# Kernel optimization log

Hardware: AMD Instinct MI355X
Metric: run time of the kernel (lower is better)

## Reference

```python
import jax, jax.numpy as jnp
import numpy as np

C = 512
NUM_HEADS = 8
GROUPS = 32
EPS_GN = 1e-5
EPS_ATTN = 1e-6


def setup_inputs() -> dict:
    key = jax.random.key(0)
    ks = jax.random.split(key, 7)
    B, H, W = 8, 64, 64
    x = jax.random.normal(ks[0], (B, C, H, W), dtype=jnp.float32)
    # GroupNorm affine (torch default: weight=1, bias=0)
    norm_gamma = jnp.ones((C,), dtype=jnp.float32)
    norm_beta = jnp.zeros((C,), dtype=jnp.float32)
    # 1x1 conv weights stored as (out, in); torch Conv2d kaiming-ish scale
    qkv_w = jax.random.normal(ks[1], (3 * C, C), dtype=jnp.float32) * (1.0 / np.sqrt(C))
    qkv_b = jax.random.normal(ks[2], (3 * C,), dtype=jnp.float32) * 0.01
    proj_w = jax.random.normal(ks[3], (C, C), dtype=jnp.float32) * (1.0 / np.sqrt(C))
    proj_b = jax.random.normal(ks[4], (C,), dtype=jnp.float32) * 0.01
    return {"x": x, "norm_gamma": norm_gamma, "norm_beta": norm_beta,
            "qkv_w": qkv_w, "qkv_b": qkv_b, "proj_w": proj_w, "proj_b": proj_b}


def _group_norm(x, gamma, beta):
    B, Cc, H, W = x.shape
    xg = x.reshape(B, GROUPS, Cc // GROUPS, H, W)
    mean = xg.mean(axis=(2, 3, 4), keepdims=True)
    var = xg.var(axis=(2, 3, 4), keepdims=True)
    xn = (xg - mean) * jax.lax.rsqrt(var + EPS_GN)
    xn = xn.reshape(B, Cc, H, W)
    return xn * gamma[None, :, None, None] + beta[None, :, None, None]


def reference(x, norm_gamma, norm_beta, qkv_w, qkv_b, proj_w, proj_b):
    B, Cc, H, W = x.shape
    h, d = NUM_HEADS, Cc // NUM_HEADS
    N = H * W
    x_norm = _group_norm(x, norm_gamma, norm_beta)
    # 1x1 conv == channel GEMM
    qkv = jnp.einsum('bchw,oc->bohw', x_norm, qkv_w) + qkv_b[None, :, None, None]
    q, k, v = jnp.split(qkv, 3, axis=1)
    # (B, C, H, W) -> (B, h, N, d)
    def to_heads(t):
        return t.reshape(B, h, d, N).transpose(0, 1, 3, 2)
    q, k, v = to_heads(q), to_heads(k), to_heads(v)
    # phi(x) = elu(x) + 1
    q = jax.nn.elu(q) + 1.0
    k = jax.nn.elu(k) + 1.0
    kv = jnp.einsum('bhnd,bhne->bhde', k, v)          # (B,h,d,d)
    out = jnp.einsum('bhnd,bhde->bhne', q, kv)        # (B,h,N,d)
    denom = jnp.einsum('bhnd,bhd->bhn', q, k.sum(axis=2))
    out = out / (denom[..., None] + EPS_ATTN)
    # (B,h,N,d) -> (B,C,H,W)
    attn = out.transpose(0, 1, 3, 2).reshape(B, Cc, H, W)
    proj = jnp.einsum('bchw,oc->bohw', attn, proj_w) + proj_b[None, :, None, None]
    # dropout is identity at inference
    return x + proj
```

## Files before the change

### kernel.cpp

```cpp
#include <hip/hip_runtime.h>
#include <math.h>

#define BATCH   8
#define CCH     512
#define NHEADS  8
#define HD      64
#define NGROUPS 32
#define CPG     16
#define NSP     4096
#define O1      1536

typedef __attribute__((ext_vector_type(8))) short          short8;
typedef __attribute__((ext_vector_type(8))) unsigned short ushort8;
typedef __attribute__((ext_vector_type(4))) unsigned short ushort4v;
typedef __attribute__((ext_vector_type(4))) float          float4v;

#define GLOAD_LDS16(g, s) __builtin_amdgcn_global_load_lds(                   \
    (const __attribute__((address_space(1))) void*)(g),                       \
    (__attribute__((address_space(3))) void*)(s), 16, 0, 0)

__device__ __forceinline__ float phi_act(float v) {
    return v > 0.f ? v + 1.f : __expf(v);
}
__device__ __forceinline__ unsigned short f2bf(float f) {
    union { float f; unsigned int u; } c; c.f = f;
    unsigned int u = c.u;
    u += 0x7fffu + ((u >> 16) & 1u);
    return (unsigned short)(u >> 16);
}
__device__ __forceinline__ float bf2f(unsigned short s) {
    union { unsigned int u; float f; } c; c.u = ((unsigned int)s) << 16;
    return c.f;
}


__global__ __launch_bounds__(256) void pre_kernel(const float* __restrict__ x,
                                                  const float* __restrict__ gamma,
                                                  const float* __restrict__ beta,
                                                  const float* __restrict__ qw,
                                                  const float* __restrict__ pw,
                                                  unsigned short* __restrict__ qwb,
                                                  unsigned short* __restrict__ pwb,
                                                  float* __restrict__ ksum,
                                                  float* __restrict__ ss) {
    __shared__ float r1[256], r2[256];
    const int bid = blockIdx.x;
    const int t   = threadIdx.x;
    if (bid < 1024) {
        int i = (bid * 256 + t) * 4;
        if (i < O1 * CCH) {
            float4 v = *(const float4*)(qw + i);
            unsigned short o[4] = {f2bf(v.x), f2bf(v.y), f2bf(v.z), f2bf(v.w)};
            *(uint2*)(qwb + i) = *(uint2*)o;
        } else {
            int j = i - O1 * CCH;
            float4 v = *(const float4*)(pw + j);
            unsigned short o[4] = {f2bf(v.x), f2bf(v.y), f2bf(v.z), f2bf(v.w)};
            *(uint2*)(pwb + j) = *(uint2*)o;
        }
        if (bid == 0) {
            float4 z = {0.f, 0.f, 0.f, 0.f};
            #pragma unroll
            for (int l = 0; l < 4; ++l)
                *(float4*)(ksum + (l * 256 + t) * 4) = z;
        }
        return;
    }
    const int bg = bid - 1024;
    const float* base = x + (size_t)bg * (CPG * NSP);
    float s = 0.f, s2 = 0.f;
    #pragma unroll 4
    for (int i = 0; i < 64; ++i) {
        float4 v = *(const float4*)(base + (i * 256 + t) * 4);
        s  += v.x + v.y + v.z + v.w;
        s2 += v.x * v.x + v.y * v.y + v.z * v.z + v.w * v.w;
    }
    r1[t] = s; r2[t] = s2;
    __syncthreads();
    for (int off = 128; off > 0; off >>= 1) {
        if (t < off) { r1[t] += r1[t + off]; r2[t] += r2[t + off]; }
        __syncthreads();
    }
    if (t < CPG) {
        const float inv = 1.f / 65536.f;
        float mean = r1[0] * inv;
        float var  = r2[0] * inv - mean * mean;
        float rstd = rsqrtf(var + 1e-5f);
        int b = bg / NGROUPS, g = bg % NGROUPS;
        int c = g * CPG + t;
        float sc = gamma[c] * rstd;
        float sh = beta[c] - mean * sc;
        ss[(b * CCH + c) * 2]     = sc;
        ss[(b * CCH + c) * 2 + 1] = sh;
    }
}

__global__ __launch_bounds__(256) void xnT_kernel(const float* __restrict__ x,
                                                  const float* __restrict__ ss,
                                                  unsigned short* __restrict__ xnT) {
    const int n0 = blockIdx.x * 64, c0 = blockIdx.y * 64, b = blockIdx.z;
    const int t = threadIdx.x;
    __shared__ float tile[64][65];
    const float* xb  = x + ((size_t)b * CCH + c0) * NSP + n0;
    const float* ssb = ss + b * CCH * 2;

    const int lr = t / 16, lc = (t % 16) * 4;
    #pragma unroll
    for (int j = 0; j < 4; ++j) {
        int cr = j * 16 + lr;
        float4 v = *(const float4*)(xb + (size_t)cr * NSP + lc);
        float sc = ssb[(c0 + cr) * 2], sh = ssb[(c0 + cr) * 2 + 1];
        tile[cr][lc + 0] = v.x * sc + sh;
        tile[cr][lc + 1] = v.y * sc + sh;
        tile[cr][lc + 2] = v.z * sc + sh;
        tile[cr][lc + 3] = v.w * sc + sh;
    }
    __syncthreads();
    #pragma unroll
    for (int j = 0; j < 2; ++j) {
        int wd = j * 256 + t;
        int n  = wd >> 3;
        int cb = (wd & 7) * 8;
        ushort8 o;
        #pragma unroll
        for (int i = 0; i < 8; ++i) o[i] = f2bf(tile[cb + i][n]);
        *(ushort8*)(xnT + ((size_t)b * NSP + n0 + n) * CCH + c0 + cb) = o;
    }
}

__global__ __launch_bounds__(256) void gemm_qkv(const unsigned short* __restrict__ A,
                                                const unsigned short* __restrict__ Bt,
                                                const float* __restrict__ bias,
                                                unsigned short* __restrict__ qT,
                                                float* __restrict__ ksum,
                                                float* __restrict__ kvp) {
    const int n0 = blockIdx.x * 128;
    const int b  = blockIdx.z;
    const int t  = threadIdx.x;
    const int wv = t >> 6, ln = t & 63;
    const int quad = ln >> 4, lm = ln & 15;
    const int wo = (wv >> 1) * 64, wn = (wv & 1) * 64;

    __shared__ __align__(16) unsigned short sh[16384];

    float4v acc[4][4];
    #pragma unroll
    for (int i = 0; i < 4; ++i)
        #pragma unroll
        for (int j = 0; j < 4; ++j) acc[i][j] = {0.f, 0.f, 0.f, 0.f};

    const unsigned short* bBase = Bt + ((size_t)b * NSP + n0) * CCH;
    const int srow = ln >> 2;
    const int scol = ((ln & 3) ^ ((ln >> 3) & 3)) * 8;
    const int slab0 = wv * 2, slab1 = slab0 + 1;
    const int dA0 = slab0 * 512, dA1 = slab1 * 512;
    const int sc  = (quad ^ ((lm >> 1) & 3)) * 8;

    if (blockIdx.y < 8) {
        const int h = blockIdx.y;
        const unsigned short* aK = A + (size_t)(512 + h * 64) * CCH;
        const unsigned short* aV = A + (size_t)(1024 + h * 64) * CCH;
        const unsigned short* aR0 = ((slab0 < 4)
            ? aK + (size_t)(slab0 * 16 + srow) * CCH
            : aV + (size_t)((slab0 - 4) * 16 + srow) * CCH) + scol;
        const unsigned short* aR1 = ((slab1 < 4)
            ? aK + (size_t)(slab1 * 16 + srow) * CCH
            : aV + (size_t)((slab1 - 4) * 16 + srow) * CCH) + scol;
        const unsigned short* bR0 = bBase + (size_t)(slab0 * 16 + srow) * CCH + scol;
        const unsigned short* bR1 = bBase + (size_t)(slab1 * 16 + srow) * CCH + scol;

        GLOAD_LDS16(aR0, sh + dA0);
        GLOAD_LDS16(aR1, sh + dA1);
        GLOAD_LDS16(bR0, sh + 4096 + dA0);
        GLOAD_LDS16(bR1, sh + 4096 + dA1);
        __syncthreads();

        int cur = 0;
        for (int step = 0; step < 15; ++step) {
            const int nb = (cur ^ 1) * 8192;
            const int k1 = (step + 1) * 32;
            GLOAD_LDS16(aR0 + k1, sh + nb + dA0);
            GLOAD_LDS16(aR1 + k1, sh + nb + dA1);
            GLOAD_LDS16(bR0 + k1, sh + nb + 4096 + dA0);
            GLOAD_LDS16(bR1 + k1, sh + nb + 4096 + dA1);
            const unsigned short* Ab = sh + cur * 8192;
            const unsigned short* Bb = Ab + 4096;
            short8 fw[4], fx[4];
            #pragma unroll
            for (int i = 0; i < 4; ++i)
                fw[i] = *(const short8*)(Ab + (wo + i * 16 + lm) * 32 + sc);
            #pragma unroll
            for (int j = 0; j < 4; ++j)
                fx[j] = *(const short8*)(Bb + (wn + j * 16 + lm) * 32 + sc);
            #pragma unroll
            for (int i = 0; i < 4; ++i)
                #pragma unroll
                for (int j = 0; j < 4; ++j)
                    acc[i][j] = __builtin_amdgcn_mfma_f32_16x16x32_bf16(
                        fx[j], fw[i], acc[i][j], 0, 0, 0);
            __syncthreads();
            cur ^= 1;
        }
        {
            const unsigned short* Ab = sh + cur * 8192;
            const unsigned short* Bb = Ab + 4096;
            short8 fw[4], fx[4];
            #pragma unroll
            for (int i = 0; i < 4; ++i)
                fw[i] = *(const short8*)(Ab + (wo + i * 16 + lm) * 32 + sc);
            #pragma unroll
            for (int j = 0; j < 4; ++j)
                fx[j] = *(const short8*)(Bb + (wn + j * 16 + lm) * 32 + sc);
            #pragma unroll
            for (int i = 0; i < 4; ++i)
                #pragma unroll
                for (int j = 0; j < 4; ++j)
                    acc[i][j] = __builtin_amdgcn_mfma_f32_16x16x32_bf16(
                        fx[j], fw[i], acc[i][j], 0, 0, 0);
        }

        __syncthreads();
        const bool isk = (wv < 2);
        const float* bptr = bias + (isk ? 512 : 1024) + h * 64;
        float ksp[4] = {0.f, 0.f, 0.f, 0.f};
        #pragma unroll
        for (int i = 0; i < 4; ++i) {
            float bs = bptr[i * 16 + lm];
            int row = wo + i * 16 + lm;
            #pragma unroll
            for (int j = 0; j < 4; ++j) {
                int n = wn + j * 16 + quad * 4;
                ushort4v pk;
                #pragma unroll
                for (int r = 0; r < 4; ++r) {
                    float v = acc[i][j][r] + bs;
                    if (isk) { v = phi_act(v); ksp[i] += v; }
                    pk[r] = f2bf(v);
                }
                int idx = row * 128 + ((((n >> 3) ^ (row & 15)) << 3) | (n & 7));
                *(ushort4v*)(sh + idx) = pk;
            }
        }
        if (isk) {
            #pragma unroll
            for (int i = 0; i < 4; ++i) {
                float s = ksp[i];
                s += __shfl_xor(s, 16);
                s += __shfl_xor(s, 32);
                if (quad == 0)
                    atomicAdd(ksum + b * CCH + h * 64 + i * 16 + lm, s);
            }
        }
        __syncthreads();

        const int wd = (wv >> 1) * 32, we = (wv & 1) * 32;
        float4v acc2[2][2];
        #pragma unroll
        for (int i = 0; i < 2; ++i)
            #pragma unroll
            for (int j = 0; j < 2; ++j) acc2[i][j] = {0.f, 0.f, 0.f, 0.f};

        #pragma unroll
        for (int ks = 0; ks < 4; ++ks) {
            short8 ka[2], vbf[2];
            #pragma unroll
            for (int i2 = 0; i2 < 2; ++i2) {
                int row = wd + i2 * 16 + lm;
                ka[i2] = *(const short8*)(sh + row * 128 +
                                          (((ks * 4 + quad) ^ (row & 15)) << 3));
            }
            #pragma unroll
            for (int j2 = 0; j2 < 2; ++j2) {
                int row = 64 + we + j2 * 16 + lm;
                vbf[j2] = *(const short8*)(sh + row * 128 +
                                           (((ks * 4 + quad) ^ (row & 15)) << 3));
            }
            #pragma unroll
            for (int i2 = 0; i2 < 2; ++i2)
                #pragma unroll
                for (int j2 = 0; j2 < 2; ++j2)
                    acc2[i2][j2] = __builtin_amdgcn_mfma_f32_16x16x32_bf16(
                        vbf[j2], ka[i2], acc2[i2][j2], 0, 0, 0);
        }

        const int chunk = blockIdx.x;
        const int bh = b * 8 + h;
        #pragma unroll
        for (int i2 = 0; i2 < 2; ++i2)
            #pragma unroll
            for (int j2 = 0; j2 < 2; ++j2) {
                int d = wd + i2 * 16 + lm;
                int e = we + j2 * 16 + quad * 4;
                float4 r = {acc2[i2][j2][0], acc2[i2][j2][1],
                            acc2[i2][j2][2], acc2[i2][j2][3]};
                *(float4*)(kvp + ((size_t)(chunk * 64 + bh) * 64 + d) * 64 + e) = r;
            }
    } else {
        const int o0 = (blockIdx.y - 8) * 128;
        const unsigned short* aBase = A + (size_t)o0 * CCH;
        const unsigned short* aR0 = aBase + (size_t)(slab0 * 16 + srow) * CCH + scol;
        const unsigned short* aR1 = aBase + (size_t)(slab1 * 16 + srow) * CCH + scol;
        const unsigned short* bR0 = bBase + (size_t)(slab0 * 16 + srow) * CCH + scol;
        const unsigned short* bR1 = bBase + (size_t)(slab1 * 16 + srow) * CCH + scol;

        GLOAD_LDS16(aR0, sh + dA0);
        GLOAD_LDS16(aR1, sh + dA1);
        GLOAD_LDS16(bR0, sh + 4096 + dA0);
        GLOAD_LDS16(bR1, sh + 4096 + dA1);
        __syncthreads();

        int cur = 0;
        for (int step = 0; step < 15; ++step) {
            const int nb = (cur ^ 1) * 8192;
            const int k1 = (step + 1) * 32;
            GLOAD_LDS16(aR0 + k1, sh + nb + dA0);
            GLOAD_LDS16(aR1 + k1, sh + nb + dA1);
            GLOAD_LDS16(bR0 + k1, sh + nb + 4096 + dA0);
            GLOAD_LDS16(bR1 + k1, sh + nb + 4096 + dA1);
            const unsigned short* Ab = sh + cur * 8192;
            const unsigned short* Bb = Ab + 4096;
            short8 fw[4], fx[4];
            #pragma unroll
            for (int i = 0; i < 4; ++i)
                fw[i] = *(const short8*)(Ab + (wo + i * 16 + lm) * 32 + sc);
            #pragma unroll
            for (int j = 0; j < 4; ++j)
                fx[j] = *(const short8*)(Bb + (wn + j * 16 + lm) * 32 + sc);
            #pragma unroll
            for (int i = 0; i < 4; ++i)
                #pragma unroll
                for (int j = 0; j < 4; ++j)
                    acc[i][j] = __builtin_amdgcn_mfma_f32_16x16x32_bf16(
                        fw[i], fx[j], acc[i][j], 0, 0, 0);
            __syncthreads();
            cur ^= 1;
        }
        {
            const unsigned short* Ab = sh + cur * 8192;
            const unsigned short* Bb = Ab + 4096;
            short8 fw[4], fx[4];
            #pragma unroll
            for (int i = 0; i < 4; ++i)
                fw[i] = *(const short8*)(Ab + (wo + i * 16 + lm) * 32 + sc);
            #pragma unroll
            for (int j = 0; j < 4; ++j)
                fx[j] = *(const short8*)(Bb + (wn + j * 16 + lm) * 32 + sc);
            #pragma unroll
            for (int i = 0; i < 4; ++i)
                #pragma unroll
                for (int j = 0; j < 4; ++j)
                    acc[i][j] = __builtin_amdgcn_mfma_f32_16x16x32_bf16(
                        fw[i], fx[j], acc[i][j], 0, 0, 0);
        }

        #pragma unroll
        for (int i = 0; i < 4; ++i) {
            int ob = o0 + wo + i * 16 + quad * 4;
            float4 b4 = *(const float4*)(bias + ob);
            float bs[4] = {b4.x, b4.y, b4.z, b4.w};
            #pragma unroll
            for (int j = 0; j < 4; ++j) {
                int n = n0 + wn + j * 16 + lm;
                ushort4v pk;
                #pragma unroll
                for (int r = 0; r < 4; ++r)
                    pk[r] = f2bf(phi_act(acc[i][j][r] + bs[r]));
                *(ushort4v*)(qT + ((size_t)b * NSP + n) * CCH + ob) = pk;
            }
        }
    }
}

__global__ __launch_bounds__(256) void post_kernel(const float* __restrict__ kvp,
                                                   const unsigned short* __restrict__ pwb,
                                                   const unsigned short* __restrict__ qT,
                                                   const float* __restrict__ ksum,
                                                   unsigned short* __restrict__ Mw,
                                                   float* __restrict__ den) {
    const int t = threadIdx.x;
    __shared__ __align__(16) unsigned short kvs[64 * 64];

    if (blockIdx.x < 64) {
        const int bh = blockIdx.x;
        const int b = bh >> 3, h = bh & 7;
        const int wv = t >> 6, ln = t & 63;
        const int quad = ln >> 4, lm = ln & 15;

        {
            const int d = t >> 2, e0 = (t & 3) * 16;
            float4 s0 = {0.f, 0.f, 0.f, 0.f}, s1 = s0, s2 = s0, s3 = s0;
            for (int p = 0; p < 32; ++p) {
                const float* src = kvp + ((size_t)(p * 64 + bh) * 64 + d) * 64 + e0;
                float4 v0 = *(const float4*)(src);
                float4 v1 = *(const float4*)(src + 4);
                float4 v2 = *(const float4*)(src + 8);
                float4 v3 = *(const float4*)(src + 12);
                s0.x += v0.x; s0.y += v0.y; s0.z += v0.z; s0.w += v0.w;
                s1.x += v1.x; s1.y += v1.y; s1.z += v1.z; s1.w += v1.w;
                s2.x += v2.x; s2.y += v2.y; s2.z += v2.z; s2.w += v2.w;
                s3.x += v3.x; s3.y += v3.y; s3.z += v3.z; s3.w += v3.w;
            }
            ushort8 o0 = {f2bf(s0.x), f2bf(s0.y), f2bf(s0.z), f2bf(s0.w),
                          f2bf(s1.x), f2bf(s1.y), f2bf(s1.z), f2bf(s1.w)};
            ushort8 o1 = {f2bf(s2.x), f2bf(s2.y), f2bf(s2.z), f2bf(s2.w),
                          f2bf(s3.x), f2bf(s3.y), f2bf(s3.z), f2bf(s3.w)};
            int c0 = e0 >> 3;
            *(ushort8*)(kvs + d * 64 + ((c0 ^ (d & 7)) << 3))       = o0;
            *(ushort8*)(kvs + d * 64 + (((c0 + 1) ^ (d & 7)) << 3)) = o1;
        }
        __syncthreads();

        short8 ka[4][2];
        #pragma unroll
        for (int i = 0; i < 4; ++i)
            #pragma unroll
            for (int kk = 0; kk < 2; ++kk) {
                int d = i * 16 + lm;
                ka[i][kk] = *(const short8*)(kvs + d * 64 +
                            (((kk * 4 + quad) ^ (lm & 7)) << 3));
            }
        for (int half = 0; half < 2; ++half) {
            const int ob = half * 256 + wv * 64;
            short8 fw[4][2];
            #pragma unroll
            for (int j = 0; j < 4; ++j)
                #pragma unroll
                for (int kk = 0; kk < 2; ++kk) {
                    int o = ob + j * 16 + lm;
                    fw[j][kk] = *(const short8*)(pwb + (size_t)o * CCH + h * 64 +
                                                 kk * 32 + quad * 8);
                }
            float4v acc[4][4];
            #pragma unroll
            for (int i = 0; i < 4; ++i)
                #pragma unroll
                for (int j = 0; j < 4; ++j) acc[i][j] = {0.f, 0.f, 0.f, 0.f};
            #pragma unroll
            for (int kk = 0; kk < 2; ++kk)
                #pragma unroll
                for (int i = 0; i < 4; ++i)
                    #pragma unroll
                    for (int j = 0; j < 4; ++j)
                        acc[i][j] = __builtin_amdgcn_mfma_f32_16x16x32_bf16(
                            ka[i][kk], fw[j][kk], acc[i][j], 0, 0, 0);
            #pragma unroll
            for (int i = 0; i < 4; ++i)
                #pragma unroll
                for (int j = 0; j < 4; ++j) {
                    int o = ob + j * 16 + lm;
                    int c = h * 64 + i * 16 + quad * 4;
                    ushort4v pk;
                    #pragma unroll
                    for (int r = 0; r < 4; ++r) pk[r] = f2bf(acc[i][j][r]);
                    *(ushort4v*)(Mw + ((size_t)b * CCH + o) * CCH + c) = pk;
                }
        }
        return;
    }

    const int bid = blockIdx.x - 64;
    const int b  = bid >> 5;
    const int n0 = (bid & 31) * 128;
    const int wv = t >> 6, ln = t & 63;
    float kf[8];
    #pragma unroll
    for (int l = 0; l < 8; ++l) kf[l] = ksum[b * CCH + ln * 8 + l];
    #pragma unroll 4
    for (int it = 0; it < 32; ++it) {
        int n = n0 + wv * 32 + it;
        short8 qv = *(const short8*)(qT + ((size_t)b * NSP + n) * CCH + ln * 8);
        float s = 0.f;
        #pragma unroll
        for (int l = 0; l < 8; ++l)
            s += bf2f((unsigned short)qv[l]) * kf[l];
        #pragma unroll
        for (int off = 1; off < 64; off <<= 1) s += __shfl_xor(s, off);
        if (ln == 0) den[(size_t)b * NSP + n] = s;
    }
}

__global__ __launch_bounds__(256) void gemm_proj(const unsigned short* __restrict__ Mw,
                                                 const unsigned short* __restrict__ Bt,
                                                 const float* __restrict__ bias,
                                                 const float* __restrict__ den,
                                                 const float* __restrict__ resid,
                                                 float* __restrict__ outF) {
    const int n0 = blockIdx.x * 128;
    const int o0 = blockIdx.y * 128;
    const int b  = blockIdx.z;
    const int t  = threadIdx.x;
    const int wv = t >> 6, ln = t & 63;
    const int quad = ln >> 4, lm = ln & 15;
    const int wo = (wv >> 1) * 64, wn = (wv & 1) * 64;

    __shared__ __align__(16) unsigned short sh[16384];

    float4v acc[4][4];
    #pragma unroll
    for (int i = 0; i < 4; ++i)
        #pragma unroll
        for (int j = 0; j < 4; ++j) acc[i][j] = {0.f, 0.f, 0.f, 0.f};

    const unsigned short* aBase = Mw + ((size_t)b * CCH + o0) * CCH;
    const unsigned short* bBase = Bt + ((size_t)b * NSP + n0) * CCH;

    const int srow = ln >> 2;
    const int scol = ((ln & 3) ^ ((ln >> 3) & 3)) * 8;
    const int slab0 = wv * 2, slab1 = slab0 + 1;
    const unsigned short* aR0 = aBase + (size_t)(slab0 * 16 + srow) * CCH + scol;
    const unsigned short* aR1 = aBase + (size_t)(slab1 * 16 + srow) * CCH + scol;
    const unsigned short* bR0 = bBase + (size_t)(slab0 * 16 + srow) * CCH + scol;
    const unsigned short* bR1 = bBase + (size_t)(slab1 * 16 + srow) * CCH + scol;
    const int dA0 = slab0 * 512, dA1 = slab1 * 512;
    const int sc  = (quad ^ ((lm >> 1) & 3)) * 8;

    GLOAD_LDS16(aR0, sh + dA0);
    GLOAD_LDS16(aR1, sh + dA1);
    GLOAD_LDS16(bR0, sh + 4096 + dA0);
    GLOAD_LDS16(bR1, sh + 4096 + dA1);
    __syncthreads();

    int cur = 0;
    for (int step = 0; step < 15; ++step) {
        const int nb = (cur ^ 1) * 8192;
        const int k1 = (step + 1) * 32;
        GLOAD_LDS16(aR0 + k1, sh + nb + dA0);
        GLOAD_LDS16(aR1 + k1, sh + nb + dA1);
        GLOAD_LDS16(bR0 + k1, sh + nb + 4096 + dA0);
        GLOAD_LDS16(bR1 + k1, sh + nb + 4096 + dA1);
        const unsigned short* Ab = sh + cur * 8192;
        const unsigned short* Bb = Ab + 4096;
        short8 fw[4], fx[4];
        #pragma unroll
        for (int i = 0; i < 4; ++i)
            fw[i] = *(const short8*)(Ab + (wo + i * 16 + lm) * 32 + sc);
        #pragma unroll
        for (int j = 0; j < 4; ++j)
            fx[j] = *(const short8*)(Bb + (wn + j * 16 + lm) * 32 + sc);
        #pragma unroll
        for (int i = 0; i < 4; ++i)
            #pragma unroll
            for (int j = 0; j < 4; ++j)
                acc[i][j] = __builtin_amdgcn_mfma_f32_16x16x32_bf16(
                    fx[j], fw[i], acc[i][j], 0, 0, 0);
        __syncthreads();
        cur ^= 1;
    }
    {
        const unsigned short* Ab = sh + cur * 8192;
        const unsigned short* Bb = Ab + 4096;
        short8 fw[4], fx[4];
        #pragma unroll
        for (int i = 0; i < 4; ++i)
            fw[i] = *(const short8*)(Ab + (wo + i * 16 + lm) * 32 + sc);
        #pragma unroll
        for (int j = 0; j < 4; ++j)
            fx[j] = *(const short8*)(Bb + (wn + j * 16 + lm) * 32 + sc);
        #pragma unroll
        for (int i = 0; i < 4; ++i)
            #pragma unroll
            for (int j = 0; j < 4; ++j)
                acc[i][j] = __builtin_amdgcn_mfma_f32_16x16x32_bf16(
                    fx[j], fw[i], acc[i][j], 0, 0, 0);
    }

    float4v rden[4];
    #pragma unroll
    for (int j = 0; j < 4; ++j) {
        float4 dn = *(const float4*)(den + (size_t)b * NSP + n0 + wn +
                                     j * 16 + quad * 4);
        rden[j][0] = 1.f / (dn.x + 1e-6f);
        rden[j][1] = 1.f / (dn.y + 1e-6f);
        rden[j][2] = 1.f / (dn.z + 1e-6f);
        rden[j][3] = 1.f / (dn.w + 1e-6f);
    }
    #pragma unroll
    for (int i = 0; i < 4; ++i) {
        int o = o0 + wo + i * 16 + lm;
        float bs = bias[o];
        #pragma unroll
        for (int j = 0; j < 4; ++j) {
            int n = n0 + wn + j * 16 + quad * 4;
            size_t off = ((size_t)b * CCH + o) * NSP + n;
            float4 rv = *(const float4*)(resid + off);
            float4 w = {acc[i][j][0] * rden[j][0] + bs + rv.x,
                        acc[i][j][1] * rden[j][1] + bs + rv.y,
                        acc[i][j][2] * rden[j][2] + bs + rv.z,
                        acc[i][j][3] * rden[j][3] + bs + rv.w};
            *(float4*)(outF + off) = w;
        }
    }
}

extern "C" void kernel_launch(void* const* d_in, const int* in_sizes, int n_in,
                              void* d_out, int out_size, void* d_ws, size_t ws_size,
                              hipStream_t stream) {
    const float* x      = (const float*)d_in[0];
    const float* gamma  = (const float*)d_in[1];
    const float* beta   = (const float*)d_in[2];
    const float* qkv_w  = (const float*)d_in[3];
    const float* qkv_b  = (const float*)d_in[4];
    const float* proj_w = (const float*)d_in[5];
    const float* proj_b = (const float*)d_in[6];
    float* out = (float*)d_out;

    float* ws   = (float*)d_ws;
    float* ss   = ws;
    float* ksum = ss + 8192;
    float* den  = ksum + 4096;
    float* kvp  = den + 32768;
    unsigned short* xnT  = (unsigned short*)(kvp + (size_t)32 * 64 * 64 * 64);
    unsigned short* qT   = xnT + (size_t)BATCH * NSP * CCH;
    unsigned short* Mw   = qT  + (size_t)BATCH * NSP * CCH;
    unsigned short* wqb  = Mw + (size_t)BATCH * CCH * CCH;
    unsigned short* wpb  = wqb + (size_t)O1 * CCH;

    pre_kernel<<<1280, 256, 0, stream>>>(x, gamma, beta, qkv_w, proj_w,
                                         wqb, wpb, ksum, ss);
    xnT_kernel<<<dim3(NSP / 64, CCH / 64, BATCH), 256, 0, stream>>>(x, ss, xnT);

    gemm_qkv<<<dim3(NSP / 128, 12, BATCH), 256, 0, stream>>>(
        wqb, xnT, qkv_b, qT, ksum, kvp);

    post_kernel<<<320, 256, 0, stream>>>(kvp, wpb, qT, ksum, Mw, den);

    gemm_proj<<<dim3(NSP / 128, CCH / 128, BATCH), 256, 0, stream>>>(
        Mw, qT, proj_b, den, x, out);
}
```

Measured before the change: 276.1 us.

## Fuse denominator dot product into projection GEMM; split post_kernel by output half

The per-position denominator (q·ksum) is now computed inside gemm_proj from the q tiles already staged in LDS, with cross-lane shuffles to reduce and broadcast it. This removes the separate den pass in post_kernel, which re-read all of qT, along with the den buffer. post_kernel now only builds the KV-projection matrix, using 128 blocks that each handle one output half instead of 64 blocks looping over both. Each half-block recomputes the kvp reduction, doubling that read, and gemm_proj gains extra VALU work and redundant denominator computation across the four o-tile blocks.

```diff
diff --git a/kernel.cpp b/kernel.cpp
--- a/kernel.cpp
+++ b/kernel.cpp
@@ -373,116 +373,89 @@
 
 __global__ __launch_bounds__(256) void post_kernel(const float* __restrict__ kvp,
                                                    const unsigned short* __restrict__ pwb,
-                                                   const unsigned short* __restrict__ qT,
-                                                   const float* __restrict__ ksum,
-                                                   unsigned short* __restrict__ Mw,
-                                                   float* __restrict__ den) {
+                                                   unsigned short* __restrict__ Mw) {
     const int t = threadIdx.x;
     __shared__ __align__(16) unsigned short kvs[64 * 64];
 
-    if (blockIdx.x < 64) {
-        const int bh = blockIdx.x;
-        const int b = bh >> 3, h = bh & 7;
-        const int wv = t >> 6, ln = t & 63;
-        const int quad = ln >> 4, lm = ln & 15;
-
-        {
-            const int d = t >> 2, e0 = (t & 3) * 16;
-            float4 s0 = {0.f, 0.f, 0.f, 0.f}, s1 = s0, s2 = s0, s3 = s0;
-            for (int p = 0; p < 32; ++p) {
-                const float* src = kvp + ((size_t)(p * 64 + bh) * 64 + d) * 64 + e0;
-                float4 v0 = *(const float4*)(src);
-                float4 v1 = *(const float4*)(src + 4);
-                float4 v2 = *(const float4*)(src + 8);
-                float4 v3 = *(const float4*)(src + 12);
-                s0.x += v0.x; s0.y += v0.y; s0.z += v0.z; s0.w += v0.w;
-                s1.x += v1.x; s1.y += v1.y; s1.z += v1.z; s1.w += v1.w;
-                s2.x += v2.x; s2.y += v2.y; s2.z += v2.z; s2.w += v2.w;
-                s3.x += v3.x; s3.y += v3.y; s3.z += v3.z; s3.w += v3.w;
-            }
-            ushort8 o0 = {f2bf(s0.x), f2bf(s0.y), f2bf(s0.z), f2bf(s0.w),
-                          f2bf(s1.x), f2bf(s1.y), f2bf(s1.z), f2bf(s1.w)};
-            ushort8 o1 = {f2bf(s2.x), f2bf(s2.y), f2bf(s2.z), f2bf(s2.w),
-                          f2bf(s3.x), f2bf(s3.y), f2bf(s3.z), f2bf(s3.w)};
-            int c0 = e0 >> 3;
-            *(ushort8*)(kvs + d * 64 + ((c0 ^ (d & 7)) << 3))       = o0;
-            *(ushort8*)(kvs + d * 64 + (((c0 + 1) ^ (d & 7)) << 3)) = o1;
-        }
-        __syncthreads();
-
-        short8 ka[4][2];
+    const int bh = blockIdx.x >> 1;
+    const int half = blockIdx.x & 1;
+    const int b = bh >> 3, h = bh & 7;
+    const int wv = t >> 6, ln = t & 63;
+    const int quad = ln >> 4, lm = ln & 15;
+
+    {
+        const int d = t >> 2, e0 = (t & 3) * 16;
+        float4 s0 = {0.f, 0.f, 0.f, 0.f}, s1 = s0, s2 = s0, s3 = s0;
+        for (int p = 0; p < 32; ++p) {
+            const float* src = kvp + ((size_t)(p * 64 + bh) * 64 + d) * 64 + e0;
+            float4 v0 = *(const float4*)(src);
+            float4 v1 = *(const float4*)(src + 4);
+            float4 v2 = *(const float4*)(src + 8);
+            float4 v3 = *(const float4*)(src + 12);
+            s0.x += v0.x; s0.y += v0.y; s0.z += v0.z; s0.w += v0.w;
+            s1.x += v1.x; s1.y += v1.y; s1.z += v1.z; s1.w += v1.w;
+            s2.x += v2.x; s2.y += v2.y; s2.z += v2.z; s2.w += v2.w;
+            s3.x += v3.x; s3.y += v3.y; s3.z += v3.z; s3.w += v3.w;
+        }
+        ushort8 o0 = {f2bf(s0.x), f2bf(s0.y), f2bf(s0.z), f2bf(s0.w),
+                      f2bf(s1.x), f2bf(s1.y), f2bf(s1.z), f2bf(s1.w)};
+        ushort8 o1 = {f2bf(s2.x), f2bf(s2.y), f2bf(s2.z), f2bf(s2.w),
+                      f2bf(s3.x), f2bf(s3.y), f2bf(s3.z), f2bf(s3.w)};
+        int c0 = e0 >> 3;
+        *(ushort8*)(kvs + d * 64 + ((c0 ^ (d & 7)) << 3))       = o0;
+        *(ushort8*)(kvs + d * 64 + (((c0 + 1) ^ (d & 7)) << 3)) = o1;
+    }
+    __syncthreads();
+
+    short8 ka[4][2];
+    #pragma unroll
+    for (int i = 0; i < 4; ++i)
+        #pragma unroll
+        for (int kk = 0; kk < 2; ++kk) {
+            int d = i * 16 + lm;
+            ka[i][kk] = *(const short8*)(kvs + d * 64 +
+                        (((kk * 4 + quad) ^ (lm & 7)) << 3));
+        }
+    const int ob = half * 256 + wv * 64;
+    short8 fw[4][2];
+    #pragma unroll
+    for (int j = 0; j < 4; ++j)
+        #pragma unroll
+        for (int kk = 0; kk < 2; ++kk) {
+            int o = ob + j * 16 + lm;
+            fw[j][kk] = *(const short8*)(pwb + (size_t)o * CCH + h * 64 +
+                                         kk * 32 + quad * 8);
+        }
+    float4v acc[4][4];
+    #pragma unroll
+    for (int i = 0; i < 4; ++i)
+        #pragma unroll
+        for (int j = 0; j < 4; ++j) acc[i][j] = {0.f, 0.f, 0.f, 0.f};
+    #pragma unroll
+    for (int kk = 0; kk < 2; ++kk)
         #pragma unroll
         for (int i = 0; i < 4; ++i)
             #pragma unroll
-            for (int kk = 0; kk < 2; ++kk) {
-                int d = i * 16 + lm;
-                ka[i][kk] = *(const short8*)(kvs + d * 64 +
-                            (((kk * 4 + quad) ^ (lm & 7)) << 3));
-            }
-        for (int half = 0; half < 2; ++half) {
-            const int ob = half * 256 + wv * 64;
-            short8 fw[4][2];
-            #pragma unroll
-            for (int j = 0; j < 4; ++j)
-                #pragma unroll
-                for (int kk = 0; kk < 2; ++kk) {
-                    int o = ob + j * 16 + lm;
-                    fw[j][kk] = *(const short8*)(pwb + (size_t)o * CCH + h * 64 +
-                                                 kk * 32 + quad * 8);
-                }
-            float4v acc[4][4];
-            #pragma unroll
-            for (int i = 0; i < 4; ++i)
-                #pragma unroll
-                for (int j = 0; j < 4; ++j) acc[i][j] = {0.f, 0.f, 0.f, 0.f};
-            #pragma unroll
-            for (int kk = 0; kk < 2; ++kk)
-                #pragma unroll
-                for (int i = 0; i < 4; ++i)
-                    #pragma unroll
-                    for (int j = 0; j < 4; ++j)
-                        acc[i][j] = __builtin_amdgcn_mfma_f32_16x16x32_bf16(
-                            ka[i][kk], fw[j][kk], acc[i][j], 0, 0, 0);
-            #pragma unroll
-            for (int i = 0; i < 4; ++i)
-                #pragma unroll
-                for (int j = 0; j < 4; ++j) {
-                    int o = ob + j * 16 + lm;
-                    int c = h * 64 + i * 16 + quad * 4;
-                    ushort4v pk;
-                    #pragma unroll
-                    for (int r = 0; r < 4; ++r) pk[r] = f2bf(acc[i][j][r]);
-                    *(ushort4v*)(Mw + ((size_t)b * CCH + o) * CCH + c) = pk;
-                }
-        }
-        return;
-    }
-
-    const int bid = blockIdx.x - 64;
-    const int b  = bid >> 5;
-    const int n0 = (bid & 31) * 128;
-    const int wv = t >> 6, ln = t & 63;
-    float kf[8];
-    #pragma unroll
-    for (int l = 0; l < 8; ++l) kf[l] = ksum[b * CCH + ln * 8 + l];
-    #pragma unroll 4
-    for (int it = 0; it < 32; ++it) {
-        int n = n0 + wv * 32 + it;
-        short8 qv = *(const short8*)(qT + ((size_t)b * NSP + n) * CCH + ln * 8);
-        float s = 0.f;
-        #pragma unroll
-        for (int l = 0; l < 8; ++l)
-            s += bf2f((unsigned short)qv[l]) * kf[l];
-        #pragma unroll
-        for (int off = 1; off < 64; off <<= 1) s += __shfl_xor(s, off);
-        if (ln == 0) den[(size_t)b * NSP + n] = s;
-    }
+            for (int j = 0; j < 4; ++j)
+                acc[i][j] = __builtin_amdgcn_mfma_f32_16x16x32_bf16(
+                    ka[i][kk], fw[j][kk], acc[i][j], 0, 0, 0);
+    #pragma unroll
+    for (int i = 0; i < 4; ++i)
+        #pragma unroll
+        for (int j = 0; j < 4; ++j) {
+            int o = ob + j * 16 + lm;
+            int c = h * 64 + i * 16 + quad * 4;
+            ushort4v pk;
+            #pragma unroll
+            for (int r = 0; r < 4; ++r) pk[r] = f2bf(acc[i][j][r]);
+            *(ushort4v*)(Mw + ((size_t)b * CCH + o) * CCH + c) = pk;
+        }
 }
 
 __global__ __launch_bounds__(256) void gemm_proj(const unsigned short* __restrict__ Mw,
                                                  const unsigned short* __restrict__ Bt,
                                                  const float* __restrict__ bias,
-                                                 const float* __restrict__ den,
+                                                 const float* __restrict__ ksum,
                                                  const float* __restrict__ resid,
                                                  float* __restrict__ outF) {
     const int n0 = blockIdx.x * 128;
@@ -500,9 +473,11 @@
     for (int i = 0; i < 4; ++i)
         #pragma unroll
         for (int j = 0; j < 4; ++j) acc[i][j] = {0.f, 0.f, 0.f, 0.f};
+    float den4[4] = {0.f, 0.f, 0.f, 0.f};
 
     const unsigned short* aBase = Mw + ((size_t)b * CCH + o0) * CCH;
     const unsigned short* bBase = Bt + ((size_t)b * NSP + n0) * CCH;
+    const float* kssB = ksum + b * CCH + quad * 8;
 
     const int srow = ln >> 2;
     const int scol = ((ln & 3) ^ ((ln >> 3) & 3)) * 8;
@@ -537,6 +512,16 @@
         #pragma unroll
         for (int j = 0; j < 4; ++j)
             fx[j] = *(const short8*)(Bb + (wn + j * 16 + lm) * 32 + sc);
+        {
+            float4 ka4 = *(const float4*)(kssB + step * 32);
+            float4 kb4 = *(const float4*)(kssB + step * 32 + 4);
+            float kf[8] = {ka4.x, ka4.y, ka4.z, ka4.w, kb4.x, kb4.y, kb4.z, kb4.w};
+            #pragma unroll
+            for (int j = 0; j < 4; ++j)
+                #pragma unroll
+                for (int l = 0; l < 8; ++l)
+                    den4[j] += bf2f((unsigned short)fx[j][l]) * kf[l];
+        }
         #pragma unroll
         for (int i = 0; i < 4; ++i)
             #pragma unroll
@@ -556,6 +541,16 @@
         #pragma unroll
         for (int j = 0; j < 4; ++j)
             fx[j] = *(const short8*)(Bb + (wn + j * 16 + lm) * 32 + sc);
+        {
+            float4 ka4 = *(const float4*)(kssB + 15 * 32);
+            float4 kb4 = *(const float4*)(kssB + 15 * 32 + 4);
+            float kf[8] = {ka4.x, ka4.y, ka4.z, ka4.w, kb4.x, kb4.y, kb4.z, kb4.w};
+            #pragma unroll
+            for (int j = 0; j < 4; ++j)
+                #pragma unroll
+                for (int l = 0; l < 8; ++l)
+                    den4[j] += bf2f((unsigned short)fx[j][l]) * kf[l];
+        }
         #pragma unroll
         for (int i = 0; i < 4; ++i)
             #pragma unroll
@@ -564,16 +559,18 @@
                     fx[j], fw[i], acc[i][j], 0, 0, 0);
     }
 
+    #pragma unroll
+    for (int j = 0; j < 4; ++j) {
+        den4[j] += __shfl_xor(den4[j], 16);
+        den4[j] += __shfl_xor(den4[j], 32);
+    }
     float4v rden[4];
     #pragma unroll
-    for (int j = 0; j < 4; ++j) {
-        float4 dn = *(const float4*)(den + (size_t)b * NSP + n0 + wn +
-                                     j * 16 + quad * 4);
-        rden[j][0] = 1.f / (dn.x + 1e-6f);
-        rden[j][1] = 1.f / (dn.y + 1e-6f);
-        rden[j][2] = 1.f / (dn.z + 1e-6f);
-        rden[j][3] = 1.f / (dn.w + 1e-6f);
-    }
+    for (int j = 0; j < 4; ++j)
+        #pragma unroll
+        for (int r = 0; r < 4; ++r)
+            rden[j][r] = 1.f / (__shfl(den4[j], quad * 4 + r) + 1e-6f);
+
     #pragma unroll
     for (int i = 0; i < 4; ++i) {
         int o = o0 + wo + i * 16 + lm;
@@ -607,8 +604,7 @@
     float* ws   = (float*)d_ws;
     float* ss   = ws;
     float* ksum = ss + 8192;
-    float* den  = ksum + 4096;
-    float* kvp  = den + 32768;
+    float* kvp  = ksum + 4096;
     unsigned short* xnT  = (unsigned short*)(kvp + (size_t)32 * 64 * 64 * 64);
     unsigned short* qT   = xnT + (size_t)BATCH * NSP * CCH;
     unsigned short* Mw   = qT  + (size_t)BATCH * NSP * CCH;
@@ -622,8 +618,8 @@
     gemm_qkv<<<dim3(NSP / 128, 12, BATCH), 256, 0, stream>>>(
         wqb, xnT, qkv_b, qT, ksum, kvp);
 
-    post_kernel<<<320, 256, 0, stream>>>(kvp, wpb, qT, ksum, Mw, den);
+    post_kernel<<<128, 256, 0, stream>>>(kvp, wpb, Mw);
 
     gemm_proj<<<dim3(NSP / 128, CCH / 128, BATCH), 256, 0, stream>>>(
-        Mw, qT, proj_b, den, x, out);
-}
+        Mw, qT, proj_b, ksum, x, out);
+}
```

New measurement: 276.4 us. No clear change (+0.1%).
